# Kernel tuning notes

Hardware: AMD Instinct MI355X
Metric: run time of the kernel (lower is better)

The kernel has to match this reference:

```python
import jax, jax.numpy as jnp
import numpy as np

DIM = 256
N_NODES = 2000
BATCH = 64


def _build_tree(n, seed=0):
    # Contiguous-children encoding: struct[i] = (ch_start, ch_end) or (-1,-1) for leaves.
    # Children indices are always > parent index (BFS frontier allocation).
    rng = np.random.default_rng(seed)
    struct = np.full((n, 2), -1, dtype=np.int32)
    ptr = 1
    i = 0
    while ptr < n:
        k = int(rng.integers(0, 5))
        if i + 1 >= ptr:  # keep the frontier non-empty
            k = max(k, 1)
        k = min(k, n - ptr)
        if k > 0:
            struct[i] = (ptr, ptr + k)
            ptr += k
        i += 1
    return struct


def _level_schedule(struct):
    # depth 0 = leaves; parent depth = 1 + max(child depths). Children idx > parent idx.
    n = struct.shape[0]
    depth = np.zeros(n, dtype=np.int64)
    for i in range(n - 1, -1, -1):
        s, e = struct[i]
        if s != -1:
            depth[i] = 1 + depth[s:e].max()
    return [np.nonzero(depth == d)[0] for d in range(int(depth.max()) + 1)]


def setup_inputs() -> dict:
    key = jax.random.key(0)
    ks = jax.random.split(key, 3)
    struct = _build_tree(N_NODES)
    structure = jnp.asarray(np.broadcast_to(struct, (BATCH, N_NODES, 2)).copy())
    features = jax.random.normal(ks[0], (BATCH, N_NODES, DIM), dtype=jnp.float32)
    s_in = (2.0 / (DIM + DIM)) ** 0.5        # glorot-ish scale
    s_inner = (2.0 / (3 * DIM + DIM)) ** 0.5
    W_in = jax.random.normal(ks[1], (DIM, DIM), dtype=jnp.float32) * s_in
    b_in = jnp.zeros((DIM,), jnp.float32)
    W_inner = jax.random.normal(ks[2], (3 * DIM, DIM), dtype=jnp.float32) * s_inner
    b_inner = jnp.zeros((DIM,), jnp.float32)
    return {"structure": structure, "features": features, "W_in": W_in,
            "b_in": b_in, "W_inner": W_inner, "b_inner": b_inner}


def reference(structure, features, W_in, b_in, W_inner, b_inner):
    # Tree structure (int) is a compile-time constant: derive a level schedule host-side,
    # then run one batched segment-reduction + Dense per tree level (deepest first).
    struct = np.asarray(structure[0])  # shared across batch
    levels = _level_schedule(struct)
    B, N, dim = features.shape
    state = jnp.zeros((B, N, dim), features.dtype)

    # Leaves: sigmoid Dense on own features (all features are finite/valid here).
    leaves = levels[0]
    state = state.at[:, leaves].set(jax.nn.sigmoid(features[:, leaves] @ W_in + b_in))

    for nodes in levels[1:]:
        starts, ends = struct[nodes, 0], struct[nodes, 1]
        counts = ends - starts
        child_ids = np.concatenate([np.arange(s, e) for s, e in zip(starts, ends)])
        seg = np.repeat(np.arange(len(nodes)), counts)
        L = len(nodes)
        cs = state[:, child_ids].transpose(1, 0, 2)          # [C, B, dim]
        ssum = jax.ops.segment_sum(cs, seg, num_segments=L)  # [L, B, dim]
        smin = jax.ops.segment_min(cs, seg, num_segments=L)
        feat = features[:, nodes].transpose(1, 0, 2)         # node's own feature joins pooling
        cnt = jnp.asarray(counts + 1, features.dtype)[:, None, None]
        c_mean = (ssum + feat) / cnt
        c_min = jnp.minimum(smin, feat)
        # NOTE: the source computes c_max with reduce_mean (bug) -> kept for fidelity.
        h = jnp.concatenate([c_mean, c_mean, c_min], axis=-1)  # [L, B, 3*dim]
        new = jax.nn.sigmoid(h @ W_inner + b_inner)
        state = state.at[:, nodes].set(new.transpose(1, 0, 2))

    return state[:, 0]  # just_root_output=True -> [B, dim]
```

## Files before the change

### kernel.cpp

```cpp
#include <hip/hip_runtime.h>

#define NNODES 2000
#define BATCH  64
#define DIM    256
#define BLOCK  128
#define MAXGRID 1024
#define TBLD   264

typedef __attribute__((ext_vector_type(8))) short  v8s;
typedef __attribute__((ext_vector_type(8))) __bf16 v8bf;
typedef __attribute__((ext_vector_type(4))) float  v4f;
typedef __attribute__((ext_vector_type(4))) int    v4i;

__device__ __forceinline__ short f2bf(float f) {
  unsigned u = __builtin_bit_cast(unsigned, f);
  u += 0x7FFFu + ((u >> 16) & 1u);
  return (short)(u >> 16);
}
__device__ __forceinline__ float bf2f(short s) {
  unsigned u = ((unsigned)(unsigned short)s) << 16;
  return __builtin_bit_cast(float, u);
}
__device__ __forceinline__ v4f mfma16(v8s a, v8s b, v4f c) {
  return __builtin_amdgcn_mfma_f32_16x16x32_bf16(
      __builtin_bit_cast(v8bf, a), __builtin_bit_cast(v8bf, b), c, 0, 0, 0);
}
__device__ __forceinline__ float sigmoidf(float x) {
  return __builtin_amdgcn_rcpf(1.0f + __builtin_amdgcn_exp2f(-1.4426950408889634f * x));
}

__global__ void prep_kernel(const float* __restrict__ W_in, const float* __restrict__ W_inner,
                            short* __restrict__ Wt_in, short* __restrict__ Wt_inner,
                            int* __restrict__ done) {
  int idx = blockIdx.x * blockDim.x + threadIdx.x;
  int stride = gridDim.x * blockDim.x;
  for (int i = idx; i < 256 * 256; i += stride) {
    int j = i >> 8, k = i & 255;
    Wt_in[j * 256 + k] = f2bf(W_in[k * 256 + j]);
  }
  for (int i = idx; i < 256 * 512; i += stride) {
    int j = i >> 9, k = i & 511;
    float v = W_inner[(k + 256) * 256 + j];
    if (k < 256) v += W_inner[k * 256 + j];
    Wt_inner[j * 512 + k] = f2bf(v);
  }
  for (int i = idx; i < 4 * NNODES; i += stride)
    __hip_atomic_store(&done[i], 0, __ATOMIC_RELAXED, __HIP_MEMORY_SCOPE_AGENT);
}

__launch_bounds__(BLOCK, 2)
__global__ void tree_kernel(const int* __restrict__ structure, const float* __restrict__ features,
                            const float* __restrict__ b_in, const float* __restrict__ b_inner,
                            const short* __restrict__ Wt_in, const short* __restrict__ Wt_inner,
                            short* __restrict__ state, int* done, float* __restrict__ out) {
  __shared__ short Xs[16 * 512];

  const int tid  = threadIdx.x;
  const int wave = tid >> 6;
  const int lane = tid & 63;
  const int ln15 = lane & 15;
  const int quad = lane >> 4;
  const int rl3  = ln15 & 7;

  const int rowb = tid >> 5;
  const int ch   = tid & 31;

  float bia_in[8], bia_nn[8];
  #pragma unroll
  for (int nt = 0; nt < 8; ++nt) {
    const int j = wave * 128 + nt * 16 + ln15;
    bia_in[nt] = b_in[j];
    bia_nn[nt] = b_inner[j];
  }

  for (int item = 4 * NNODES - 1 - (int)blockIdx.x; item >= 0; item -= (int)gridDim.x) {
    const int node = item >> 2;
    const int q    = item & 3;
    const int s = structure[2 * node];
    const int e = structure[2 * node + 1];
    const bool leaf = (s < 0);
    const int nc = e - s;
    const int K = leaf ? 256 : 512;
    const short* __restrict__ W = leaf ? Wt_in : Wt_inner;

    float4 pf[4][2];
    #pragma unroll
    for (int g = 0; g < 4; ++g) {
      const int b = q * 16 + rowb + 4 * g;
      const float* __restrict__ fp = features + ((size_t)b * NNODES + node) * DIM + ch * 8;
      pf[g][0] = ((const float4*)fp)[0];
      pf[g][1] = ((const float4*)fp)[1];
    }

    if (!leaf && wave == 0 && lane < nc) {
      int g = 0;
      while (__hip_atomic_load(&done[4 * (s + lane) + q],
                               __ATOMIC_RELAXED, __HIP_MEMORY_SCOPE_AGENT) == 0 &&
             g < (1 << 22)) {
        __builtin_amdgcn_s_sleep(1); ++g;
      }
    }
    __syncthreads();

    if (leaf) {
      #pragma unroll
      for (int g = 0; g < 4; ++g) {
        const int row = rowb + 4 * g;
        const int sw  = row & 7;
        const float4 f0 = pf[g][0], f1 = pf[g][1];
        v8s o;
        o[0] = f2bf(f0.x); o[1] = f2bf(f0.y); o[2] = f2bf(f0.z); o[3] = f2bf(f0.w);
        o[4] = f2bf(f1.x); o[5] = f2bf(f1.y); o[6] = f2bf(f1.z); o[7] = f2bf(f1.w);
        *(v8s*)&Xs[(row << 9) + ((ch ^ sw) << 3)] = o;
      }
    } else {
      v4i cb[4][4];
      #pragma unroll
      for (int ci = 0; ci < 4; ++ci) {
        if (ci < nc) {
          #pragma unroll
          for (int g = 0; g < 4; ++g) {
            const short* cp = state + ((size_t)(s + ci) * BATCH + q * 16 + rowb + 4 * g) * DIM + ch * 8;
            asm volatile("global_load_dwordx4 %0, %1, off sc0 sc1"
                         : "=v"(cb[ci][g]) : "v"(cp));
          }
        }
      }
      asm volatile("s_waitcnt vmcnt(0)" ::: "memory");
      __builtin_amdgcn_sched_barrier(0);

      const float inv = 1.0f / (float)(nc + 1);
      #pragma unroll
      for (int g = 0; g < 4; ++g) {
        const int row = rowb + 4 * g;
        const int sw  = row & 7;
        const float4 f0 = pf[g][0], f1 = pf[g][1];
        float sm[8] = {f0.x, f0.y, f0.z, f0.w, f1.x, f1.y, f1.z, f1.w};
        float mn[8];
        #pragma unroll
        for (int qq = 0; qq < 8; ++qq) mn[qq] = sm[qq];
        #pragma unroll
        for (int ci = 0; ci < 4; ++ci) {
          if (ci < nc) {
            const v8s cv = __builtin_bit_cast(v8s, cb[ci][g]);
            #pragma unroll
            for (int qq = 0; qq < 8; ++qq) {
              const float v = bf2f(cv[qq]);
              sm[qq] += v; mn[qq] = fminf(mn[qq], v);
            }
          }
        }
        v8s om, on;
        #pragma unroll
        for (int qq = 0; qq < 8; ++qq) { om[qq] = f2bf(sm[qq] * inv); on[qq] = f2bf(mn[qq]); }
        *(v8s*)&Xs[(row << 9) + ((ch ^ sw) << 3)]          = om;
        *(v8s*)&Xs[(row << 9) + (((ch + 32) ^ sw) << 3)]   = on;
      }
    }
    __syncthreads();

    v4f acc[8];
    #pragma unroll
    for (int nt = 0; nt < 8; ++nt) acc[nt] = v4f{0.f, 0.f, 0.f, 0.f};

    const short* __restrict__ Wp = W + (size_t)(wave * 128 + ln15) * K + quad * 8;
    const int nkc = K >> 5;
    v8s bcur[8];
    #pragma unroll
    for (int nt = 0; nt < 8; ++nt) bcur[nt] = *(const v8s*)(Wp + (size_t)nt * 16 * K);
    for (int kc = 0; kc < nkc; ++kc) {
      const int kn = (kc + 1 < nkc) ? kc + 1 : kc;
      v8s bnxt[8];
      #pragma unroll
      for (int nt = 0; nt < 8; ++nt) bnxt[nt] = *(const v8s*)(Wp + (size_t)nt * 16 * K + kn * 32);
      const v8s af = *(const v8s*)&Xs[(ln15 << 9) + (((kc * 4 + quad) ^ rl3) << 3)];
      #pragma unroll
      for (int nt = 0; nt < 8; ++nt)
        acc[nt] = mfma16(af, bcur[nt], acc[nt]);
      #pragma unroll
      for (int nt = 0; nt < 8; ++nt) bcur[nt] = bnxt[nt];
    }
    __syncthreads();

    #pragma unroll
    for (int nt = 0; nt < 8; ++nt) {
      const int j = wave * 128 + nt * 16 + ln15;
      const float bs = leaf ? bia_in[nt] : bia_nn[nt];
      #pragma unroll
      for (int r = 0; r < 4; ++r) {
        const int bb = quad * 4 + r;
        const float v = sigmoidf(acc[nt][r] + bs);
        Xs[bb * TBLD + j] = f2bf(v);
        if (node == 0) out[(q * 16 + bb) * DIM + j] = v;
      }
    }
    __syncthreads();

    #pragma unroll
    for (int g = 0; g < 4; ++g) {
      const int row = rowb + 4 * g;
      const v4i val = *(const v4i*)&Xs[row * TBLD + ch * 8];
      short* sp = state + ((size_t)node * BATCH + q * 16 + row) * DIM + ch * 8;
      asm volatile("global_store_dwordx4 %0, %1, off sc0 sc1" :: "v"(sp), "v"(val));
    }

    asm volatile("s_waitcnt vmcnt(0)" ::: "memory");
    __syncthreads();
    if (tid == 0)
      __hip_atomic_store(&done[item], 1,
                         __ATOMIC_RELAXED, __HIP_MEMORY_SCOPE_AGENT);
  }
}

extern "C" void kernel_launch(void* const* d_in, const int* in_sizes, int n_in,
                              void* d_out, int out_size, void* d_ws, size_t ws_size,
                              hipStream_t stream) {
  const int*   structure = (const int*)d_in[0];
  const float* features  = (const float*)d_in[1];
  const float* W_in      = (const float*)d_in[2];
  const float* b_in      = (const float*)d_in[3];
  const float* W_inner   = (const float*)d_in[4];
  const float* b_inner   = (const float*)d_in[5];
  float* out = (float*)d_out;

  char* ws = (char*)d_ws;
  short* state = (short*)ws;
  size_t off = (size_t)NNODES * BATCH * DIM * 2;
  short* Wt_in = (short*)(ws + off);    off += 256 * 256 * 2;
  short* Wt_inner = (short*)(ws + off); off += 512 * 256 * 2;
  int* done = (int*)(ws + off);

  prep_kernel<<<dim3(256), dim3(256), 0, stream>>>(W_in, W_inner, Wt_in, Wt_inner, done);

  static int coop_grid = 0;
  if (coop_grid == 0) {
    int nb = 0;
    hipError_t err = hipOccupancyMaxActiveBlocksPerMultiprocessor(
        &nb, reinterpret_cast<const void*>(tree_kernel), BLOCK, 0);
    if (err != hipSuccess || nb < 1) nb = 1;
    long g = (long)nb * 256;
    if (g > MAXGRID) g = MAXGRID;
    coop_grid = (int)g;
  }

  void* args[9];
  args[0] = (void*)&structure;
  args[1] = (void*)&features;
  args[2] = (void*)&b_in;
  args[3] = (void*)&b_inner;
  args[4] = (void*)&Wt_in;
  args[5] = (void*)&Wt_inner;
  args[6] = (void*)&state;
  args[7] = (void*)&done;
  args[8] = (void*)&out;
  hipLaunchCooperativeKernel((void*)tree_kernel, dim3(coop_grid), dim3(BLOCK), args, 0, stream);
}
```

Measured before the change: 472.6 us.

## Replace static item striding with dependency-driven work queue and 32-row items

```diff
diff --git a/kernel.cpp b/kernel.cpp
--- a/kernel.cpp
+++ b/kernel.cpp
@@ -4,7 +4,8 @@
 #define BATCH  64
 #define DIM    256
 #define BLOCK  128
-#define MAXGRID 1024
+#define GRID   1024
+#define NITEMS (2 * NNODES)
 #define TBLD   264
 
 typedef __attribute__((ext_vector_type(8))) short  v8s;
@@ -29,9 +30,11 @@
   return __builtin_amdgcn_rcpf(1.0f + __builtin_amdgcn_exp2f(-1.4426950408889634f * x));
 }
 
-__global__ void prep_kernel(const float* __restrict__ W_in, const float* __restrict__ W_inner,
-                            short* __restrict__ Wt_in, short* __restrict__ Wt_inner,
-                            int* __restrict__ done) {
+__global__ void prep1_kernel(const float* __restrict__ W_in, const float* __restrict__ W_inner,
+                             short* __restrict__ Wt_in, short* __restrict__ Wt_inner,
+                             const int* __restrict__ structure, int* __restrict__ parent,
+                             int* __restrict__ ccount, int* __restrict__ queue,
+                             int* __restrict__ qctl) {
   int idx = blockIdx.x * blockDim.x + threadIdx.x;
   int stride = gridDim.x * blockDim.x;
   for (int i = idx; i < 256 * 256; i += stride) {
@@ -44,16 +47,47 @@
     if (k < 256) v += W_inner[k * 256 + j];
     Wt_inner[j * 512 + k] = f2bf(v);
   }
-  for (int i = idx; i < 4 * NNODES; i += stride)
-    __hip_atomic_store(&done[i], 0, __ATOMIC_RELAXED, __HIP_MEMORY_SCOPE_AGENT);
+  for (int i = idx; i < NITEMS; i += stride)
+    __hip_atomic_store(&queue[i], -1, __ATOMIC_RELAXED, __HIP_MEMORY_SCOPE_AGENT);
+  for (int i = idx; i < NNODES; i += stride) {
+    const int s = structure[2 * i], e = structure[2 * i + 1];
+    const int nc = (s < 0) ? 0 : (e - s);
+    __hip_atomic_store(&ccount[2 * i],     nc, __ATOMIC_RELAXED, __HIP_MEMORY_SCOPE_AGENT);
+    __hip_atomic_store(&ccount[2 * i + 1], nc, __ATOMIC_RELAXED, __HIP_MEMORY_SCOPE_AGENT);
+    if (s >= 0)
+      for (int c = s; c < e; ++c) parent[c] = i;
+  }
+  if (idx == 0) {
+    __hip_atomic_store(&qctl[0], 0, __ATOMIC_RELAXED, __HIP_MEMORY_SCOPE_AGENT);
+    __hip_atomic_store(&qctl[1], 0, __ATOMIC_RELAXED, __HIP_MEMORY_SCOPE_AGENT);
+  }
+}
+
+__global__ void prep2_kernel(const int* __restrict__ structure,
+                             int* __restrict__ queue, int* __restrict__ qctl) {
+  int idx = blockIdx.x * blockDim.x + threadIdx.x;
+  int stride = gridDim.x * blockDim.x;
+  for (int i = idx; i < NNODES; i += stride) {
+    if (structure[2 * i] < 0) {
+      #pragma unroll
+      for (int h = 0; h < 2; ++h) {
+        const int slot = __hip_atomic_fetch_add(&qctl[1], 1, __ATOMIC_RELAXED, __HIP_MEMORY_SCOPE_AGENT);
+        __hip_atomic_store(&queue[slot], 2 * i + h, __ATOMIC_RELAXED, __HIP_MEMORY_SCOPE_AGENT);
+      }
+    }
+  }
 }
 
 __launch_bounds__(BLOCK, 2)
 __global__ void tree_kernel(const int* __restrict__ structure, const float* __restrict__ features,
                             const float* __restrict__ b_in, const float* __restrict__ b_inner,
                             const short* __restrict__ Wt_in, const short* __restrict__ Wt_inner,
-                            short* __restrict__ state, int* done, float* __restrict__ out) {
-  __shared__ short Xs[16 * 512];
+                            const int* __restrict__ parent,
+                            short* __restrict__ state, int* __restrict__ ccount,
+                            int* __restrict__ queue, int* __restrict__ qctl,
+                            float* __restrict__ out) {
+  __shared__ short Xs[32 * 512];
+  __shared__ int curitem;
 
   const int tid  = threadIdx.x;
   const int wave = tid >> 6;
@@ -73,9 +107,26 @@
     bia_nn[nt] = b_inner[j];
   }
 
-  for (int item = 4 * NNODES - 1 - (int)blockIdx.x; item >= 0; item -= (int)gridDim.x) {
-    const int node = item >> 2;
-    const int q    = item & 3;
+  while (true) {
+    __syncthreads();
+    if (tid == 0) {
+      int it = -1;
+      const int t = __hip_atomic_fetch_add(&qctl[0], 1, __ATOMIC_RELAXED, __HIP_MEMORY_SCOPE_AGENT);
+      if (t < NITEMS) {
+        int g = 0;
+        while ((it = __hip_atomic_load(&queue[t], __ATOMIC_RELAXED, __HIP_MEMORY_SCOPE_AGENT)) < 0 &&
+               g < (1 << 24)) {
+          __builtin_amdgcn_s_sleep(1); ++g;
+        }
+      }
+      curitem = it;
+    }
+    __syncthreads();
+    const int item = curitem;
+    if (item < 0) break;
+
+    const int node = item >> 1;
+    const int half = item & 1;
     const int s = structure[2 * node];
     const int e = structure[2 * node + 1];
     const bool leaf = (s < 0);
@@ -83,85 +134,79 @@
     const int K = leaf ? 256 : 512;
     const short* __restrict__ W = leaf ? Wt_in : Wt_inner;
 
-    float4 pf[4][2];
-    #pragma unroll
-    for (int g = 0; g < 4; ++g) {
-      const int b = q * 16 + rowb + 4 * g;
-      const float* __restrict__ fp = features + ((size_t)b * NNODES + node) * DIM + ch * 8;
-      pf[g][0] = ((const float4*)fp)[0];
-      pf[g][1] = ((const float4*)fp)[1];
-    }
-
-    if (!leaf && wave == 0 && lane < nc) {
-      int g = 0;
-      while (__hip_atomic_load(&done[4 * (s + lane) + q],
-                               __ATOMIC_RELAXED, __HIP_MEMORY_SCOPE_AGENT) == 0 &&
-             g < (1 << 22)) {
-        __builtin_amdgcn_s_sleep(1); ++g;
-      }
-    }
-    __syncthreads();
-
-    if (leaf) {
+    for (int pass = 0; pass < 2; ++pass) {
+      float4 pf[4][2];
       #pragma unroll
       for (int g = 0; g < 4; ++g) {
-        const int row = rowb + 4 * g;
-        const int sw  = row & 7;
-        const float4 f0 = pf[g][0], f1 = pf[g][1];
-        v8s o;
-        o[0] = f2bf(f0.x); o[1] = f2bf(f0.y); o[2] = f2bf(f0.z); o[3] = f2bf(f0.w);
-        o[4] = f2bf(f1.x); o[5] = f2bf(f1.y); o[6] = f2bf(f1.z); o[7] = f2bf(f1.w);
-        *(v8s*)&Xs[(row << 9) + ((ch ^ sw) << 3)] = o;
-      }
-    } else {
-      v4i cb[4][4];
-      #pragma unroll
-      for (int ci = 0; ci < 4; ++ci) {
-        if (ci < nc) {
-          #pragma unroll
-          for (int g = 0; g < 4; ++g) {
-            const short* cp = state + ((size_t)(s + ci) * BATCH + q * 16 + rowb + 4 * g) * DIM + ch * 8;
-            asm volatile("global_load_dwordx4 %0, %1, off sc0 sc1"
-                         : "=v"(cb[ci][g]) : "v"(cp));
-          }
-        }
-      }
-      asm volatile("s_waitcnt vmcnt(0)" ::: "memory");
-      __builtin_amdgcn_sched_barrier(0);
-
-      const float inv = 1.0f / (float)(nc + 1);
-      #pragma unroll
-      for (int g = 0; g < 4; ++g) {
-        const int row = rowb + 4 * g;
-        const int sw  = row & 7;
-        const float4 f0 = pf[g][0], f1 = pf[g][1];
-        float sm[8] = {f0.x, f0.y, f0.z, f0.w, f1.x, f1.y, f1.z, f1.w};
-        float mn[8];
-        #pragma unroll
-        for (int qq = 0; qq < 8; ++qq) mn[qq] = sm[qq];
+        const int b = half * 32 + pass * 16 + rowb + 4 * g;
+        const float* __restrict__ fp = features + ((size_t)b * NNODES + node) * DIM + ch * 8;
+        pf[g][0] = ((const float4*)fp)[0];
+        pf[g][1] = ((const float4*)fp)[1];
+      }
+      if (leaf) {
+        #pragma unroll
+        for (int g = 0; g < 4; ++g) {
+          const int row = pass * 16 + rowb + 4 * g;
+          const int sw  = row & 7;
+          const float4 f0 = pf[g][0], f1 = pf[g][1];
+          v8s o;
+          o[0] = f2bf(f0.x); o[1] = f2bf(f0.y); o[2] = f2bf(f0.z); o[3] = f2bf(f0.w);
+          o[4] = f2bf(f1.x); o[5] = f2bf(f1.y); o[6] = f2bf(f1.z); o[7] = f2bf(f1.w);
+          *(v8s*)&Xs[(row << 9) + ((ch ^ sw) << 3)] = o;
+        }
+      } else {
+        v4i cb[4][4];
         #pragma unroll
         for (int ci = 0; ci < 4; ++ci) {
           if (ci < nc) {
-            const v8s cv = __builtin_bit_cast(v8s, cb[ci][g]);
             #pragma unroll
-            for (int qq = 0; qq < 8; ++qq) {
-              const float v = bf2f(cv[qq]);
-              sm[qq] += v; mn[qq] = fminf(mn[qq], v);
+            for (int g = 0; g < 4; ++g) {
+              const short* cp = state +
+                  ((size_t)(s + ci) * BATCH + half * 32 + pass * 16 + rowb + 4 * g) * DIM + ch * 8;
+              asm volatile("global_load_dwordx4 %0, %1, off sc0 sc1"
+                           : "=v"(cb[ci][g]) : "v"(cp));
             }
           }
         }
-        v8s om, on;
-        #pragma unroll
-        for (int qq = 0; qq < 8; ++qq) { om[qq] = f2bf(sm[qq] * inv); on[qq] = f2bf(mn[qq]); }
-        *(v8s*)&Xs[(row << 9) + ((ch ^ sw) << 3)]          = om;
-        *(v8s*)&Xs[(row << 9) + (((ch + 32) ^ sw) << 3)]   = on;
-      }
-    }
-    __syncthreads();
-
-    v4f acc[8];
+        asm volatile("s_waitcnt vmcnt(0)" ::: "memory");
+        __builtin_amdgcn_sched_barrier(0);
+
+        const float inv = 1.0f / (float)(nc + 1);
+        #pragma unroll
+        for (int g = 0; g < 4; ++g) {
+          const int row = pass * 16 + rowb + 4 * g;
+          const int sw  = row & 7;
+          const float4 f0 = pf[g][0], f1 = pf[g][1];
+          float sm[8] = {f0.x, f0.y, f0.z, f0.w, f1.x, f1.y, f1.z, f1.w};
+          float mn[8];
+          #pragma unroll
+          for (int qq = 0; qq < 8; ++qq) mn[qq] = sm[qq];
+          #pragma unroll
+          for (int ci = 0; ci < 4; ++ci) {
+            if (ci < nc) {
+              const v8s cv = __builtin_bit_cast(v8s, cb[ci][g]);
+              #pragma unroll
+              for (int qq = 0; qq < 8; ++qq) {
+                const float v = bf2f(cv[qq]);
+                sm[qq] += v; mn[qq] = fminf(mn[qq], v);
+              }
+            }
+          }
+          v8s om, on;
+          #pragma unroll
+          for (int qq = 0; qq < 8; ++qq) { om[qq] = f2bf(sm[qq] * inv); on[qq] = f2bf(mn[qq]); }
+          *(v8s*)&Xs[(row << 9) + ((ch ^ sw) << 3)]        = om;
+          *(v8s*)&Xs[(row << 9) + (((ch + 32) ^ sw) << 3)] = on;
+        }
+      }
+    }
+    __syncthreads();
+
+    v4f acc[2][8];
     #pragma unroll
-    for (int nt = 0; nt < 8; ++nt) acc[nt] = v4f{0.f, 0.f, 0.f, 0.f};
+    for (int mt = 0; mt < 2; ++mt)
+      #pragma unroll
+      for (int nt = 0; nt < 8; ++nt) acc[mt][nt] = v4f{0.f, 0.f, 0.f, 0.f};
 
     const short* __restrict__ Wp = W + (size_t)(wave * 128 + ln15) * K + quad * 8;
     const int nkc = K >> 5;
@@ -173,10 +218,17 @@
       v8s bnxt[8];
       #pragma unroll
       for (int nt = 0; nt < 8; ++nt) bnxt[nt] = *(const v8s*)(Wp + (size_t)nt * 16 * K + kn * 32);
-      const v8s af = *(const v8s*)&Xs[(ln15 << 9) + (((kc * 4 + quad) ^ rl3) << 3)];
-      #pragma unroll
-      for (int nt = 0; nt < 8; ++nt)
-        acc[nt] = mfma16(af, bcur[nt], acc[nt]);
+      v8s af[2];
+      #pragma unroll
+      for (int mt = 0; mt < 2; ++mt) {
+        const int r = mt * 16 + ln15;
+        af[mt] = *(const v8s*)&Xs[(r << 9) + (((kc * 4 + quad) ^ rl3) << 3)];
+      }
+      #pragma unroll
+      for (int mt = 0; mt < 2; ++mt)
+        #pragma unroll
+        for (int nt = 0; nt < 8; ++nt)
+          acc[mt][nt] = mfma16(af[mt], bcur[nt], acc[mt][nt]);
       #pragma unroll
       for (int nt = 0; nt < 8; ++nt) bcur[nt] = bnxt[nt];
     }
@@ -187,28 +239,39 @@
       const int j = wave * 128 + nt * 16 + ln15;
       const float bs = leaf ? bia_in[nt] : bia_nn[nt];
       #pragma unroll
-      for (int r = 0; r < 4; ++r) {
-        const int bb = quad * 4 + r;
-        const float v = sigmoidf(acc[nt][r] + bs);
-        Xs[bb * TBLD + j] = f2bf(v);
-        if (node == 0) out[(q * 16 + bb) * DIM + j] = v;
+      for (int mt = 0; mt < 2; ++mt) {
+        #pragma unroll
+        for (int r = 0; r < 4; ++r) {
+          const int bb = mt * 16 + quad * 4 + r;
+          const float v = sigmoidf(acc[mt][nt][r] + bs);
+          Xs[bb * TBLD + j] = f2bf(v);
+          if (node == 0) out[(half * 32 + bb) * DIM + j] = v;
+        }
       }
     }
     __syncthreads();
 
     #pragma unroll
-    for (int g = 0; g < 4; ++g) {
+    for (int g = 0; g < 8; ++g) {
       const int row = rowb + 4 * g;
       const v4i val = *(const v4i*)&Xs[row * TBLD + ch * 8];
-      short* sp = state + ((size_t)node * BATCH + q * 16 + row) * DIM + ch * 8;
+      short* sp = state + ((size_t)node * BATCH + half * 32 + row) * DIM + ch * 8;
       asm volatile("global_store_dwordx4 %0, %1, off sc0 sc1" :: "v"(sp), "v"(val));
     }
 
     asm volatile("s_waitcnt vmcnt(0)" ::: "memory");
     __syncthreads();
-    if (tid == 0)
-      __hip_atomic_store(&done[item], 1,
-                         __ATOMIC_RELAXED, __HIP_MEMORY_SCOPE_AGENT);
+    if (tid == 0 && node > 0) {
+      const int p = parent[node];
+      const int old = __hip_atomic_fetch_add(&ccount[2 * p + half], -1,
+                                             __ATOMIC_RELAXED, __HIP_MEMORY_SCOPE_AGENT);
+      if (old == 1) {
+        const int slot = __hip_atomic_fetch_add(&qctl[1], 1,
+                                                __ATOMIC_RELAXED, __HIP_MEMORY_SCOPE_AGENT);
+        __hip_atomic_store(&queue[slot], 2 * p + half,
+                           __ATOMIC_RELAXED, __HIP_MEMORY_SCOPE_AGENT);
+      }
+    }
   }
 }
 
@@ -228,30 +291,16 @@
   size_t off = (size_t)NNODES * BATCH * DIM * 2;
   short* Wt_in = (short*)(ws + off);    off += 256 * 256 * 2;
   short* Wt_inner = (short*)(ws + off); off += 512 * 256 * 2;
-  int* done = (int*)(ws + off);
-
-  prep_kernel<<<dim3(256), dim3(256), 0, stream>>>(W_in, W_inner, Wt_in, Wt_inner, done);
-
-  static int coop_grid = 0;
-  if (coop_grid == 0) {
-    int nb = 0;
-    hipError_t err = hipOccupancyMaxActiveBlocksPerMultiprocessor(
-        &nb, reinterpret_cast<const void*>(tree_kernel), BLOCK, 0);
-    if (err != hipSuccess || nb < 1) nb = 1;
-    long g = (long)nb * 256;
-    if (g > MAXGRID) g = MAXGRID;
-    coop_grid = (int)g;
-  }
-
-  void* args[9];
-  args[0] = (void*)&structure;
-  args[1] = (void*)&features;
-  args[2] = (void*)&b_in;
-  args[3] = (void*)&b_inner;
-  args[4] = (void*)&Wt_in;
-  args[5] = (void*)&Wt_inner;
-  args[6] = (void*)&state;
-  args[7] = (void*)&done;
-  args[8] = (void*)&out;
-  hipLaunchCooperativeKernel((void*)tree_kernel, dim3(coop_grid), dim3(BLOCK), args, 0, stream);
-}
+  int* parent = (int*)(ws + off);       off += NNODES * 4;
+  int* ccount = (int*)(ws + off);       off += NITEMS * 4;
+  int* queue  = (int*)(ws + off);       off += NITEMS * 4;
+  int* qctl   = (int*)(ws + off);
+
+  prep1_kernel<<<dim3(256), dim3(256), 0, stream>>>(W_in, W_inner, Wt_in, Wt_inner,
+                                                    structure, parent, ccount, queue, qctl);
+  prep2_kernel<<<dim3(64), dim3(256), 0, stream>>>(structure, queue, qctl);
+
+  tree_kernel<<<dim3(GRID), dim3(BLOCK), 0, stream>>>(
+      structure, features, b_in, b_inner, Wt_in, Wt_inner, parent,
+      state, ccount, queue, qctl, out);
+}
```

After: 490.6 us. 1.04x slower.

## Partition batch by XCD with per-XCD dynamic node queues and local-coherence loads

Applied to the files above, without the earlier changes.

```diff
diff --git a/kernel.cpp b/kernel.cpp
--- a/kernel.cpp
+++ b/kernel.cpp
@@ -4,7 +4,8 @@
 #define BATCH  64
 #define DIM    256
 #define BLOCK  128
-#define MAXGRID 1024
+#define GRID   2048
+#define NXCD   8
 #define TBLD   264
 
 typedef __attribute__((ext_vector_type(8))) short  v8s;
@@ -31,7 +32,7 @@
 
 __global__ void prep_kernel(const float* __restrict__ W_in, const float* __restrict__ W_inner,
                             short* __restrict__ Wt_in, short* __restrict__ Wt_inner,
-                            int* __restrict__ done) {
+                            int* __restrict__ done, int* __restrict__ next) {
   int idx = blockIdx.x * blockDim.x + threadIdx.x;
   int stride = gridDim.x * blockDim.x;
   for (int i = idx; i < 256 * 256; i += stride) {
@@ -44,16 +45,23 @@
     if (k < 256) v += W_inner[k * 256 + j];
     Wt_inner[j * 512 + k] = f2bf(v);
   }
-  for (int i = idx; i < 4 * NNODES; i += stride)
-    __hip_atomic_store(&done[i], 0, __ATOMIC_RELAXED, __HIP_MEMORY_SCOPE_AGENT);
+  for (int i = idx; i < NXCD * NNODES; i += stride) done[i] = 0;
+  if (idx < NXCD) next[idx] = NNODES - 1;
 }
 
 __launch_bounds__(BLOCK, 2)
 __global__ void tree_kernel(const int* __restrict__ structure, const float* __restrict__ features,
                             const float* __restrict__ b_in, const float* __restrict__ b_inner,
                             const short* __restrict__ Wt_in, const short* __restrict__ Wt_inner,
-                            short* __restrict__ state, int* done, float* __restrict__ out) {
+                            short* __restrict__ state, int* __restrict__ done,
+                            int* __restrict__ next, float* __restrict__ out) {
   __shared__ short Xs[16 * 512];
+  __shared__ int sh_node;
+
+  unsigned xcc;
+  asm volatile("s_getreg_b32 %0, hwreg(HW_REG_XCC_ID)" : "=s"(xcc));
+  const int xcd = (int)(xcc & (NXCD - 1));
+  const int b0  = xcd * 8;
 
   const int tid  = threadIdx.x;
   const int wave = tid >> 6;
@@ -62,8 +70,8 @@
   const int quad = lane >> 4;
   const int rl3  = ln15 & 7;
 
-  const int rowb = tid >> 5;
-  const int ch   = tid & 31;
+  const int prow = tid >> 4;
+  const int pc   = tid & 15;
 
   float bia_in[8], bia_nn[8];
   #pragma unroll
@@ -73,9 +81,15 @@
     bia_nn[nt] = b_inner[j];
   }
 
-  for (int item = 4 * NNODES - 1 - (int)blockIdx.x; item >= 0; item -= (int)gridDim.x) {
-    const int node = item >> 2;
-    const int q    = item & 3;
+  while (true) {
+    __syncthreads();
+    if (tid == 0)
+      sh_node = __hip_atomic_fetch_add(&next[xcd], -1,
+                                       __ATOMIC_RELAXED, __HIP_MEMORY_SCOPE_AGENT);
+    __syncthreads();
+    const int node = sh_node;
+    if (node < 0) break;
+
     const int s = structure[2 * node];
     const int e = structure[2 * node + 1];
     const bool leaf = (s < 0);
@@ -83,20 +97,16 @@
     const int K = leaf ? 256 : 512;
     const short* __restrict__ W = leaf ? Wt_in : Wt_inner;
 
-    float4 pf[4][2];
-    #pragma unroll
-    for (int g = 0; g < 4; ++g) {
-      const int b = q * 16 + rowb + 4 * g;
-      const float* __restrict__ fp = features + ((size_t)b * NNODES + node) * DIM + ch * 8;
-      pf[g][0] = ((const float4*)fp)[0];
-      pf[g][1] = ((const float4*)fp)[1];
-    }
-
-    if (!leaf && wave == 0 && lane < nc) {
+    const float* __restrict__ fp = features + ((size_t)(b0 + prow) * NNODES + node) * DIM + pc * 16;
+    float4 pf[4];
+    #pragma unroll
+    for (int q = 0; q < 4; ++q) pf[q] = ((const float4*)fp)[q];
+
+    if (!leaf && tid < nc) {
       int g = 0;
-      while (__hip_atomic_load(&done[4 * (s + lane) + q],
+      while (__hip_atomic_load(&done[xcd * NNODES + s + tid],
                                __ATOMIC_RELAXED, __HIP_MEMORY_SCOPE_AGENT) == 0 &&
-             g < (1 << 22)) {
+             g < (1 << 24)) {
         __builtin_amdgcn_s_sleep(1); ++g;
       }
     }
@@ -104,26 +114,24 @@
 
     if (leaf) {
       #pragma unroll
-      for (int g = 0; g < 4; ++g) {
-        const int row = rowb + 4 * g;
-        const int sw  = row & 7;
-        const float4 f0 = pf[g][0], f1 = pf[g][1];
+      for (int h = 0; h < 2; ++h) {
         v8s o;
-        o[0] = f2bf(f0.x); o[1] = f2bf(f0.y); o[2] = f2bf(f0.z); o[3] = f2bf(f0.w);
-        o[4] = f2bf(f1.x); o[5] = f2bf(f1.y); o[6] = f2bf(f1.z); o[7] = f2bf(f1.w);
-        *(v8s*)&Xs[(row << 9) + ((ch ^ sw) << 3)] = o;
+        #pragma unroll
+        for (int q = 0; q < 8; ++q) {
+          const float* pfa = (const float*)&pf[2 * h];
+          o[q] = f2bf(pfa[q]);
+        }
+        const int ch = pc * 2 + h;
+        *(v8s*)&Xs[(prow << 9) + ((ch ^ prow) << 3)] = o;
       }
     } else {
-      v4i cb[4][4];
+      v4i cb[4][2];
       #pragma unroll
       for (int ci = 0; ci < 4; ++ci) {
         if (ci < nc) {
-          #pragma unroll
-          for (int g = 0; g < 4; ++g) {
-            const short* cp = state + ((size_t)(s + ci) * BATCH + q * 16 + rowb + 4 * g) * DIM + ch * 8;
-            asm volatile("global_load_dwordx4 %0, %1, off sc0 sc1"
-                         : "=v"(cb[ci][g]) : "v"(cp));
-          }
+          const short* cp = state + ((size_t)(s + ci) * BATCH + b0 + prow) * DIM + pc * 16;
+          asm volatile("global_load_dwordx4 %0, %1, off sc0" : "=v"(cb[ci][0]) : "v"(cp));
+          asm volatile("global_load_dwordx4 %0, %1, off sc0" : "=v"(cb[ci][1]) : "v"(cp + 8));
         }
       }
       asm volatile("s_waitcnt vmcnt(0)" ::: "memory");
@@ -131,30 +139,28 @@
 
       const float inv = 1.0f / (float)(nc + 1);
       #pragma unroll
-      for (int g = 0; g < 4; ++g) {
-        const int row = rowb + 4 * g;
-        const int sw  = row & 7;
-        const float4 f0 = pf[g][0], f1 = pf[g][1];
-        float sm[8] = {f0.x, f0.y, f0.z, f0.w, f1.x, f1.y, f1.z, f1.w};
-        float mn[8];
-        #pragma unroll
-        for (int qq = 0; qq < 8; ++qq) mn[qq] = sm[qq];
+      for (int h = 0; h < 2; ++h) {
+        const float* pfa = (const float*)&pf[2 * h];
+        float sm[8], mn[8];
+        #pragma unroll
+        for (int q = 0; q < 8; ++q) { sm[q] = pfa[q]; mn[q] = pfa[q]; }
         #pragma unroll
         for (int ci = 0; ci < 4; ++ci) {
           if (ci < nc) {
-            const v8s cv = __builtin_bit_cast(v8s, cb[ci][g]);
+            const v8s cv = __builtin_bit_cast(v8s, cb[ci][h]);
             #pragma unroll
-            for (int qq = 0; qq < 8; ++qq) {
-              const float v = bf2f(cv[qq]);
-              sm[qq] += v; mn[qq] = fminf(mn[qq], v);
+            for (int q = 0; q < 8; ++q) {
+              const float v = bf2f(cv[q]);
+              sm[q] += v; mn[q] = fminf(mn[q], v);
             }
           }
         }
         v8s om, on;
         #pragma unroll
-        for (int qq = 0; qq < 8; ++qq) { om[qq] = f2bf(sm[qq] * inv); on[qq] = f2bf(mn[qq]); }
-        *(v8s*)&Xs[(row << 9) + ((ch ^ sw) << 3)]          = om;
-        *(v8s*)&Xs[(row << 9) + (((ch + 32) ^ sw) << 3)]   = on;
+        for (int q = 0; q < 8; ++q) { om[q] = f2bf(sm[q] * inv); on[q] = f2bf(mn[q]); }
+        const int ch = pc * 2 + h;
+        *(v8s*)&Xs[(prow << 9) + ((ch ^ prow) << 3)]        = om;
+        *(v8s*)&Xs[(prow << 9) + (((ch + 32) ^ prow) << 3)] = on;
       }
     }
     __syncthreads();
@@ -186,28 +192,29 @@
     for (int nt = 0; nt < 8; ++nt) {
       const int j = wave * 128 + nt * 16 + ln15;
       const float bs = leaf ? bia_in[nt] : bia_nn[nt];
-      #pragma unroll
-      for (int r = 0; r < 4; ++r) {
-        const int bb = quad * 4 + r;
-        const float v = sigmoidf(acc[nt][r] + bs);
-        Xs[bb * TBLD + j] = f2bf(v);
-        if (node == 0) out[(q * 16 + bb) * DIM + j] = v;
-      }
-    }
-    __syncthreads();
-
-    #pragma unroll
-    for (int g = 0; g < 4; ++g) {
-      const int row = rowb + 4 * g;
-      const v4i val = *(const v4i*)&Xs[row * TBLD + ch * 8];
-      short* sp = state + ((size_t)node * BATCH + q * 16 + row) * DIM + ch * 8;
-      asm volatile("global_store_dwordx4 %0, %1, off sc0 sc1" :: "v"(sp), "v"(val));
-    }
-
+      if (quad < 2) {
+        #pragma unroll
+        for (int r = 0; r < 4; ++r) {
+          const int bb = quad * 4 + r;
+          const float v = sigmoidf(acc[nt][r] + bs);
+          Xs[bb * TBLD + j] = f2bf(v);
+          if (node == 0) out[(b0 + bb) * DIM + j] = v;
+        }
+      }
+    }
+    __syncthreads();
+
+    {
+      const v4i v0 = *(const v4i*)&Xs[prow * TBLD + pc * 16];
+      const v4i v1 = *(const v4i*)&Xs[prow * TBLD + pc * 16 + 8];
+      short* sp = state + ((size_t)node * BATCH + b0 + prow) * DIM + pc * 16;
+      *(v4i*)sp = v0;
+      *(v4i*)(sp + 8) = v1;
+    }
     asm volatile("s_waitcnt vmcnt(0)" ::: "memory");
     __syncthreads();
     if (tid == 0)
-      __hip_atomic_store(&done[item], 1,
+      __hip_atomic_store(&done[xcd * NNODES + node], 1,
                          __ATOMIC_RELAXED, __HIP_MEMORY_SCOPE_AGENT);
   }
 }
@@ -228,30 +235,12 @@
   size_t off = (size_t)NNODES * BATCH * DIM * 2;
   short* Wt_in = (short*)(ws + off);    off += 256 * 256 * 2;
   short* Wt_inner = (short*)(ws + off); off += 512 * 256 * 2;
-  int* done = (int*)(ws + off);
-
-  prep_kernel<<<dim3(256), dim3(256), 0, stream>>>(W_in, W_inner, Wt_in, Wt_inner, done);
-
-  static int coop_grid = 0;
-  if (coop_grid == 0) {
-    int nb = 0;
-    hipError_t err = hipOccupancyMaxActiveBlocksPerMultiprocessor(
-        &nb, reinterpret_cast<const void*>(tree_kernel), BLOCK, 0);
-    if (err != hipSuccess || nb < 1) nb = 1;
-    long g = (long)nb * 256;
-    if (g > MAXGRID) g = MAXGRID;
-    coop_grid = (int)g;
-  }
-
-  void* args[9];
-  args[0] = (void*)&structure;
-  args[1] = (void*)&features;
-  args[2] = (void*)&b_in;
-  args[3] = (void*)&b_inner;
-  args[4] = (void*)&Wt_in;
-  args[5] = (void*)&Wt_inner;
-  args[6] = (void*)&state;
-  args[7] = (void*)&done;
-  args[8] = (void*)&out;
-  hipLaunchCooperativeKernel((void*)tree_kernel, dim3(coop_grid), dim3(BLOCK), args, 0, stream);
-}
+  int* done = (int*)(ws + off);         off += NXCD * NNODES * 4;
+  int* next = (int*)(ws + off);
+
+  prep_kernel<<<dim3(256), dim3(256), 0, stream>>>(W_in, W_inner, Wt_in, Wt_inner,
+                                                   done, next);
+  tree_kernel<<<dim3(GRID), dim3(BLOCK), 0, stream>>>(
+      structure, features, b_in, b_inner, Wt_in, Wt_inner,
+      state, done, next, out);
+}
```

Result: slower. 595.8 us (+26.1%).
